# Kernel tuning notes

Hardware: AMD Instinct MI355X
Metric: run time of the kernel (lower is better)

Reference implementation:

```python
import jax, jax.numpy as jnp
import numpy as np

B, S, H = 4, 1024, 1024
R = 512          # num_rules
M = 1024         # memory_size
HEADS = 16
STEPS = 3        # inference_steps
TEMP = 1.0       # softmax_temperature
LN_EPS = 1e-5


def setup_inputs() -> dict:
    key = jax.random.key(0)
    ks = jax.random.split(key, 40)
    std = 0.02
    p = lambda k, shp: (jax.random.normal(k, shp, jnp.float32) * std)
    inp = {
        "hidden_states": jax.random.normal(ks[0], (B, S, H), jnp.float32),
        "rule_embeddings": p(ks[1], (R, H)),
        "rule_sel_w": p(ks[2], (H, R)), "rule_sel_b": jnp.zeros((R,), jnp.float32),
        # self-attention (nn.MultiheadAttention) projections
        "attn_wq": p(ks[3], (H, H)), "attn_bq": jnp.zeros((H,), jnp.float32),
        "attn_wk": p(ks[4], (H, H)), "attn_bk": jnp.zeros((H,), jnp.float32),
        "attn_wv": p(ks[5], (H, H)), "attn_bv": jnp.zeros((H,), jnp.float32),
        "attn_wo": p(ks[6], (H, H)), "attn_bo": jnp.zeros((H,), jnp.float32),
        # memory bank + key/query/value projections
        "memory": p(ks[7], (M, H)),
        "mem_q_w": p(ks[8], (H, H)), "mem_q_b": jnp.zeros((H,), jnp.float32),
        "mem_k_w": p(ks[9], (H, H)), "mem_k_b": jnp.zeros((H,), jnp.float32),
        "mem_v_w": p(ks[10], (H, H)), "mem_v_b": jnp.zeros((H,), jnp.float32),
        # memory_attention (nn.MultiheadAttention) projections
        "mattn_wq": p(ks[11], (H, H)), "mattn_bq": jnp.zeros((H,), jnp.float32),
        "mattn_wk": p(ks[12], (H, H)), "mattn_bk": jnp.zeros((H,), jnp.float32),
        "mattn_wv": p(ks[13], (H, H)), "mattn_bv": jnp.zeros((H,), jnp.float32),
        "mattn_wo": p(ks[14], (H, H)), "mattn_bo": jnp.zeros((H,), jnp.float32),
        # rule_application: Linear(2H,H)+LN+GELU+Linear(H,H)
        "ra_w1": p(ks[15], (2 * H, H)), "ra_b1": jnp.zeros((H,), jnp.float32),
        "ra_ln_s": jnp.ones((H,), jnp.float32), "ra_ln_b": jnp.zeros((H,), jnp.float32),
        "ra_w2": p(ks[16], (H, H)), "ra_b2": jnp.zeros((H,), jnp.float32),
        # confidence_scorer
        "conf_w": p(ks[17], (H, 1)), "conf_b": jnp.zeros((1,), jnp.float32),
    }
    return inp


def _mha(q_in, k_in, v_in, wq, bq, wk, bk, wv, bv, wo, bo):
    # standard nn.MultiheadAttention math (batch_first, eval mode -> no dropout)
    b, sq, h = q_in.shape
    d = h // HEADS
    qh = (q_in @ wq + bq).reshape(b, sq, HEADS, d)
    kh = (k_in @ wk + bk).reshape(b, -1, HEADS, d)
    vh = (v_in @ wv + bv).reshape(b, -1, HEADS, d)
    scores = jnp.einsum('bqhd,bkhd->bhqk', qh, kh) / jnp.sqrt(jnp.asarray(d, qh.dtype))
    probs = jax.nn.softmax(scores, axis=-1)
    out = jnp.einsum('bhqk,bkhd->bqhd', probs, vh).reshape(b, sq, h)
    return out @ wo + bo


def _ln(x, s, b):
    mu = x.mean(-1, keepdims=True)
    var = ((x - mu) ** 2).mean(-1, keepdims=True)
    return (x - mu) / jnp.sqrt(var + LN_EPS) * s + b


def reference(hidden_states, rule_embeddings, rule_sel_w, rule_sel_b,
              attn_wq, attn_bq, attn_wk, attn_bk, attn_wv, attn_bv, attn_wo, attn_bo,
              memory, mem_q_w, mem_q_b, mem_k_w, mem_k_b, mem_v_w, mem_v_b,
              mattn_wq, mattn_bq, mattn_wk, mattn_bk, mattn_wv, mattn_bv, mattn_wo, mattn_bo,
              ra_w1, ra_b1, ra_ln_s, ra_ln_b, ra_w2, ra_b2, conf_w, conf_b):
    h = hidden_states
    b = h.shape[0]
    # memory keys/values are input-independent: project once, broadcast over batch
    mk = jnp.broadcast_to((memory @ mem_k_w + mem_k_b)[None], (b, M, H))
    mv = jnp.broadcast_to((memory @ mem_v_w + mem_v_b)[None], (b, M, H))
    for _ in range(STEPS):
        # rule routing: soft selection over the rule-embedding table
        rule_probs = jax.nn.softmax((h @ rule_sel_w + rule_sel_b) / TEMP, axis=-1)  # [B,S,R]
        selected = jnp.einsum('bsr,rh->bsh', rule_probs, rule_embeddings)           # [B,S,H]
        # self-attention reasoning
        h = h + _mha(h, h, h, attn_wq, attn_bq, attn_wk, attn_bk,
                     attn_wv, attn_bv, attn_wo, attn_bo)
        # memory attention
        mq = h @ mem_q_w + mem_q_b
        h = h + _mha(mq, mk, mv, mattn_wq, mattn_bq, mattn_wk, mattn_bk,
                     mattn_wv, mattn_bv, mattn_wo, mattn_bo)
        # rule application MLP on [h ; selected_rules]
        x = jnp.concatenate([h, selected], axis=-1)                                  # [B,S,2H]
        u = jax.nn.gelu(_ln(x @ ra_w1 + ra_b1, ra_ln_s, ra_ln_b), approximate=False)
        h = h + (u @ ra_w2 + ra_b2)
    confidence = jax.nn.sigmoid(h @ conf_w + conf_b)  # [B,S,1]
    return h, confidence
```

## Files before the change

kernel.cpp:

```cpp
#include <hip/hip_runtime.h>
#include <stdint.h>

typedef _Float16 f16;
typedef __attribute__((ext_vector_type(4))) float floatx4;
typedef __attribute__((ext_vector_type(8))) f16   f16x8;
typedef __attribute__((ext_vector_type(4))) f16   f16x4;

#define GLD_LDS16(gp, lp)                                                                      \
  __builtin_amdgcn_global_load_lds((const __attribute__((address_space(1))) void*)(uintptr_t)(gp), \
                                   (__attribute__((address_space(3))) void*)(uintptr_t)(lp), 16, 0, 0)

struct SrlOut {
  int n0;
  const float* bias;
  const float* resid;
  float* Cf; f16* Cb;
  int ldcf, ldcb, transV;
  long long sCb, sCh;
};
struct SrlGemmArgs {
  const f16* A; const f16* B;
  int M, N, K, lda, ldb;
  long long sAb, sAh, sBb, sBh;
  float alpha;
  int nOuts;
  SrlOut out[4];
};

template<int BM, int BN, int MINW>
__global__ __launch_bounds__(256, MINW) void srl_gemm(SrlGemmArgs g) {
  constexpr int BK = 64;
  constexpr int ACH = BM / 32;
  constexpr int BCH = BN / 32;
  constexpr int MI  = (BM == 128 && BN == 128) ? 4 : 2;
  constexpr int NI  = (BN == 128) ? 4 : ((BM == 128) ? 4 : 2);
  __shared__ f16 As[BM * BK];
  __shared__ f16 Bs[BN * BK];
  const int tid  = threadIdx.x;
  const int wid  = tid >> 6;
  const int lane = tid & 63;
  const int z  = blockIdx.z, zh = z & 15, zb = z >> 4;

  const int gx = gridDim.x;
  const int NT = gx * gridDim.y;
  const int L  = blockIdx.y * gx + blockIdx.x;
  const int W  = ((NT & 7) == 0) ? ((L & 7) * (NT >> 3) + (L >> 3)) : L;
  const int tn = (W % gx) * BN;
  const int tm = (W / gx) * BM;

  const f16* Ab = g.A + (long long)zb * g.sAb + (long long)zh * g.sAh + (long long)tm * g.lda;
  const f16* Bb = g.B + (long long)zb * g.sBb + (long long)zh * g.sBh + (long long)tn * g.ldb;
  const int maxAr = g.M - 1 - tm;
  const int maxBr = g.N - 1 - tn;

  int aR[ACH], aO[ACH];
#pragma unroll
  for (int i = 0; i < ACH; ++i) {
    int e = wid * (BM * 16) + i * 512 + lane * 8;
    int r = e >> 6, s = (e >> 3) & 7;
    aR[i] = r; aO[i] = ((s - r) & 7) * 8;
  }
  int bR[BCH], bO[BCH];
#pragma unroll
  for (int i = 0; i < BCH; ++i) {
    int e = wid * (BN * 16) + i * 512 + lane * 8;
    int r = e >> 6, s = (e >> 3) & 7;
    bR[i] = r; bO[i] = ((s - r) & 7) * 8;
  }
  f16* lA = As + wid * (BM * 16);
  f16* lB = Bs + wid * (BN * 16);

  floatx4 acc[MI][NI];
#pragma unroll
  for (int a = 0; a < MI; ++a)
#pragma unroll
    for (int b = 0; b < NI; ++b) {
      acc[a][b][0] = 0.f; acc[a][b][1] = 0.f; acc[a][b][2] = 0.f; acc[a][b][3] = 0.f;
    }

  const int wm = (BM == 128 && BN == 128) ? (wid & 1) * 64
               : (BN == 128)              ? 0
               : (BM == 128)              ? wid * 32
                                          : (wid & 1) * 32;
  const int wn = (BM == 128 && BN == 128) ? (wid >> 1) * 64
               : (BM == 64 && BN == 64)   ? (wid >> 1) * 32
                                          : 0;
  const int lm = lane & 15;
  const int quad = lane >> 4;

  for (int k0 = 0; k0 < g.K; k0 += BK) {
    __syncthreads();
#pragma unroll
    for (int i = 0; i < ACH; ++i) {
      int r = aR[i] <= maxAr ? aR[i] : maxAr;
      GLD_LDS16(Ab + (long long)r * g.lda + (k0 + aO[i]), lA + i * 512);
    }
#pragma unroll
    for (int i = 0; i < BCH; ++i) {
      int r = bR[i] <= maxBr ? bR[i] : maxBr;
      GLD_LDS16(Bb + (long long)r * g.ldb + (k0 + bO[i]), lB + i * 512);
    }
    __syncthreads();
#pragma unroll
    for (int ks = 0; ks < 2; ++ks) {
      f16x8 af[MI], bfr[NI];
#pragma unroll
      for (int mi = 0; mi < MI; ++mi) {
        int row = wm + mi * 16 + lm;
        int sg = ((ks * 4 + quad) + row) & 7;
        af[mi] = *(const f16x8*)(As + row * 64 + sg * 8);
      }
#pragma unroll
      for (int ni = 0; ni < NI; ++ni) {
        int row = wn + ni * 16 + lm;
        int sg = ((ks * 4 + quad) + row) & 7;
        bfr[ni] = *(const f16x8*)(Bs + row * 64 + sg * 8);
      }
#pragma unroll
      for (int mi = 0; mi < MI; ++mi)
#pragma unroll
        for (int ni = 0; ni < NI; ++ni)
          acc[mi][ni] = __builtin_amdgcn_mfma_f32_16x16x32_f16(af[mi], bfr[ni], acc[mi][ni], 0, 0, 0);
    }
  }

  int oi = 0;
  for (int j = 1; j < g.nOuts; ++j)
    if (tn >= g.out[j].n0) oi = j;
  const SrlOut O = g.out[oi];
  const long long zc = (long long)zb * O.sCb + (long long)zh * O.sCh;
#pragma unroll
  for (int mi = 0; mi < MI; ++mi) {
#pragma unroll
    for (int r = 0; r < 4; ++r) {
      int m = tm + wm + mi * 16 + quad * 4 + r;
      if (m >= g.M) continue;
#pragma unroll
      for (int ni = 0; ni < NI; ++ni) {
        int n = tn + wn + ni * 16 + lm;
        if (n >= g.N) continue;
        int nl = n - O.n0;
        float v = acc[mi][ni][r] * g.alpha;
        if (O.bias)  v += O.bias[nl];
        if (O.resid) v += O.resid[(long long)m * O.ldcf + nl];
        if (O.Cf)    O.Cf[zc + (long long)m * O.ldcf + nl] = v;
        if (O.Cb) {
          long long idx = O.transV
              ? ((long long)(m >> 10) * 1048576 + (long long)nl * 1024 + (m & 1023))
              : (zc + (long long)m * O.ldcb + nl);
          O.Cb[idx] = (f16)v;
        }
      }
    }
  }
}

struct SrlFlashArgs {
  const f16* Q; const f16* K; const f16* VT; f16* O;
  long long sQb, sKb, sVb;
  float scale;
};

__global__ __launch_bounds__(256, 2) void srl_flash(SrlFlashArgs a) {
  __shared__ f16 Qs[8192];
  __shared__ f16 Ks[8192];
  __shared__ f16 VTs[8192];
  __shared__ f16 Ps[4][4096];
  const int tid = threadIdx.x, wid = tid >> 6, lane = tid & 63;
  const int quad = lane >> 4, c = lane & 15;
  const int L = blockIdx.x;
  const int bh = (L & 7) + ((L >> 6) << 3);
  const int qt = (L >> 3) & 7;
  const int b = bh >> 4, h = bh & 15;
  const f16* Qg = a.Q + (long long)b * a.sQb + (long long)qt * 131072 + h * 64;
  const f16* Kg = a.K + (long long)b * a.sKb + h * 64;
  const f16* Vg = a.VT + (long long)b * a.sVb + (long long)h * 65536;
  f16* Og = a.O + (long long)b * 1048576 + (long long)qt * 131072 + h * 64;

  int rRow[4], rOff[4];
#pragma unroll
  for (int i = 0; i < 4; ++i) {
    int e = wid * 2048 + i * 512 + lane * 8;
    int r = e >> 6, gL = (e >> 3) & 7;
    rRow[i] = r; rOff[i] = ((gL - r) & 7) * 8;
  }
  int vRow[4], vOff[4];
#pragma unroll
  for (int i = 0; i < 4; ++i) {
    int e = wid * 2048 + i * 512 + lane * 8;
    int d = e >> 7, gL = (e >> 3) & 15;
    vRow[i] = d; vOff[i] = ((gL - (d & 7)) & 15) * 8;
  }

#pragma unroll
  for (int i = 0; i < 4; ++i)
    GLD_LDS16(Qg + (long long)rRow[i] * 1024 + rOff[i], Qs + wid * 2048 + i * 512);
  __syncthreads();

  const int wq = wid * 32;
  f16x8 qf[2][2];
#pragma unroll
  for (int nf = 0; nf < 2; ++nf)
#pragma unroll
    for (int ch = 0; ch < 2; ++ch) {
      int row = wq + nf * 16 + c;
      int slot = ((ch * 4 + quad) + row) & 7;
      f16x8 v = *(const f16x8*)(Qs + row * 64 + slot * 8);
      f16 sc = (f16)a.scale;
#pragma unroll
      for (int j = 0; j < 8; ++j) v[j] = v[j] * sc;
      qf[nf][ch] = v;
    }

  float l_s[2] = {0.f, 0.f};
  floatx4 Oa[2][4];
#pragma unroll
  for (int nf = 0; nf < 2; ++nf)
#pragma unroll
    for (int no = 0; no < 4; ++no) {
      Oa[nf][no][0] = 0.f; Oa[nf][no][1] = 0.f; Oa[nf][no][2] = 0.f; Oa[nf][no][3] = 0.f;
    }

  for (int t = 0; t < 8; ++t) {
    __syncthreads();
#pragma unroll
    for (int i = 0; i < 4; ++i)
      GLD_LDS16(Kg + (long long)(t * 128 + rRow[i]) * 1024 + rOff[i], Ks + wid * 2048 + i * 512);
#pragma unroll
    for (int i = 0; i < 4; ++i)
      GLD_LDS16(Vg + (long long)vRow[i] * 1024 + (t * 128 + vOff[i]), VTs + wid * 2048 + i * 512);
    __syncthreads();

    floatx4 sT[2][8];
#pragma unroll
    for (int nf = 0; nf < 2; ++nf)
#pragma unroll
      for (int mf = 0; mf < 8; ++mf) {
        sT[nf][mf][0] = 0.f; sT[nf][mf][1] = 0.f; sT[nf][mf][2] = 0.f; sT[nf][mf][3] = 0.f;
      }
#pragma unroll
    for (int ch = 0; ch < 2; ++ch)
#pragma unroll
      for (int mf = 0; mf < 8; ++mf) {
        int key = mf * 16 + c;
        int slot = ((ch * 4 + quad) + key) & 7;
        f16x8 kf = *(const f16x8*)(Ks + key * 64 + slot * 8);
        sT[0][mf] = __builtin_amdgcn_mfma_f32_16x16x32_f16(kf, qf[0][ch], sT[0][mf], 0, 0, 0);
        sT[1][mf] = __builtin_amdgcn_mfma_f32_16x16x32_f16(kf, qf[1][ch], sT[1][mf], 0, 0, 0);
      }

#pragma unroll
    for (int nf = 0; nf < 2; ++nf) {
      float lt = 0.f;
      const int q = nf * 16 + c;
#pragma unroll
      for (int mf = 0; mf < 8; ++mf) {
        f16x4 pk;
#pragma unroll
        for (int r = 0; r < 4; ++r) {
          float p = __builtin_amdgcn_exp2f(sT[nf][mf][r]);
          lt += p;
          pk[r] = (f16)p;
        }
        int kg = mf * 2 + (quad >> 1), sub = (quad & 1) * 4;
        int slot = (kg + (q & 7)) & 15;
        *(f16x4*)(Ps[wid] + q * 128 + slot * 8 + sub) = pk;
      }
      lt += __shfl_xor(lt, 16);
      lt += __shfl_xor(lt, 32);
      l_s[nf] += lt;
    }
#pragma unroll
    for (int cc = 0; cc < 4; ++cc) {
      f16x8 af[2];
#pragma unroll
      for (int nf = 0; nf < 2; ++nf) {
        int q = nf * 16 + c;
        int slot = ((cc * 4 + quad) + (q & 7)) & 15;
        af[nf] = *(const f16x8*)(Ps[wid] + q * 128 + slot * 8);
      }
#pragma unroll
      for (int no = 0; no < 4; ++no) {
        int d = no * 16 + c;
        int slot = ((cc * 4 + quad) + (d & 7)) & 15;
        f16x8 vf = *(const f16x8*)(VTs + d * 128 + slot * 8);
        Oa[0][no] = __builtin_amdgcn_mfma_f32_16x16x32_f16(af[0], vf, Oa[0][no], 0, 0, 0);
        Oa[1][no] = __builtin_amdgcn_mfma_f32_16x16x32_f16(af[1], vf, Oa[1][no], 0, 0, 0);
      }
    }
  }

#pragma unroll
  for (int nf = 0; nf < 2; ++nf)
#pragma unroll
    for (int r = 0; r < 4; ++r) {
      float li = 1.f / __shfl(l_s[nf], quad * 4 + r);
      int qrow = wq + nf * 16 + quad * 4 + r;
#pragma unroll
      for (int no = 0; no < 4; ++no)
        Qs[qrow * 64 + no * 16 + c] = (f16)(Oa[nf][no][r] * li);
    }
  __syncthreads();
#pragma unroll
  for (int i = 0; i < 4; ++i) {
    int e = wid * 2048 + i * 512 + lane * 8;
    int row = e >> 6, col = e & 63;
    *(f16x8*)(Og + (long long)row * 1024 + col) = *(const f16x8*)(Qs + e);
  }
}

__global__ __launch_bounds__(256) void srl_softmax_rule(const float* logits, f16* probs) {
  __shared__ float red[16];
  const long long row = blockIdx.x;
  const float* p = logits + row * 512;
  const int tid = threadIdx.x;
  float v0 = p[tid], v1 = p[tid + 256];
  float mx = fmaxf(v0, v1);
#pragma unroll
  for (int o = 32; o > 0; o >>= 1) mx = fmaxf(mx, __shfl_down(mx, o));
  const int wid = tid >> 6, lane = tid & 63;
  if (lane == 0) red[wid] = mx;
  __syncthreads();
  if (tid == 0) red[8] = fmaxf(fmaxf(red[0], red[1]), fmaxf(red[2], red[3]));
  __syncthreads();
  mx = red[8];
  float e0 = __expf(v0 - mx), e1 = __expf(v1 - mx);
  float s = e0 + e1;
#pragma unroll
  for (int o = 32; o > 0; o >>= 1) s += __shfl_down(s, o);
  if (lane == 0) red[wid + 4] = s;
  __syncthreads();
  if (tid == 0) red[9] = 1.f / (red[4] + red[5] + red[6] + red[7]);
  __syncthreads();
  const float inv = red[9];
  probs[row * 512 + tid] = (f16)(e0 * inv);
  probs[row * 512 + tid + 256] = (f16)(e1 * inv);
}

__global__ __launch_bounds__(256) void srl_ln_gelu(const float* x, const float* gam, const float* bet, f16* out) {
  __shared__ float red[16];
  const long long row = blockIdx.x;
  const float* p = x + row * 1024;
  const int tid = threadIdx.x;
  float4 xv = *(const float4*)(p + tid * 4);
  float v[4] = {xv.x, xv.y, xv.z, xv.w};
  float s = v[0] + v[1] + v[2] + v[3];
  float s2 = v[0] * v[0] + v[1] * v[1] + v[2] * v[2] + v[3] * v[3];
#pragma unroll
  for (int o = 32; o > 0; o >>= 1) { s += __shfl_down(s, o); s2 += __shfl_down(s2, o); }
  const int wid = tid >> 6, lane = tid & 63;
  if (lane == 0) { red[wid] = s; red[wid + 4] = s2; }
  __syncthreads();
  if (tid == 0) {
    float ts = red[0] + red[1] + red[2] + red[3];
    float ts2 = red[4] + red[5] + red[6] + red[7];
    float mu = ts * (1.f / 1024.f);
    float var = ts2 * (1.f / 1024.f) - mu * mu;
    red[8] = mu;
    red[9] = rsqrtf(var + 1e-5f);
  }
  __syncthreads();
  const float mu = red[8], rstd = red[9];
  f16x4 o4;
#pragma unroll
  for (int i = 0; i < 4; ++i) {
    int c = tid * 4 + i;
    float t = (v[i] - mu) * rstd * gam[c] + bet[c];
    float ge = 0.5f * t * (1.f + erff(t * 0.70710678118654752f));
    o4[i] = (f16)ge;
  }
  *(f16x4*)(out + row * 1024 + tid * 4) = o4;
}

struct SrlTcEnt { const float* src; f16* dst; int rows, cols, trans, tileStart; };
struct SrlTcArgs { SrlTcEnt e[16]; };

__global__ __launch_bounds__(256) void srl_convert_weights(SrlTcArgs a) {
  __shared__ float t[32][33];
  const int bt = blockIdx.x;
  int ei = 0;
#pragma unroll
  for (int j = 1; j < 16; ++j)
    if (bt >= a.e[j].tileStart) ei = j;
  SrlTcEnt E = a.e[ei];
  const int lt = bt - E.tileStart;
  const int tcols = E.cols >> 5;
  const int tr = lt / tcols;
  const int tc = lt - tr * tcols;
  const int r = threadIdx.x >> 5;
  const int c = threadIdx.x & 31;
  if (!E.trans) {
#pragma unroll
    for (int p = 0; p < 4; ++p) {
      long long rr = tr * 32 + r + p * 8;
      long long idx = rr * E.cols + tc * 32 + c;
      E.dst[idx] = (f16)E.src[idx];
    }
  } else {
#pragma unroll
    for (int p = 0; p < 4; ++p)
      t[r + p * 8][c] = E.src[(long long)(tr * 32 + r + p * 8) * E.cols + tc * 32 + c];
    __syncthreads();
#pragma unroll
    for (int p = 0; p < 4; ++p)
      E.dst[(long long)(tc * 32 + r + p * 8) * E.rows + tr * 32 + c] = (f16)t[c][r + p * 8];
  }
}

__global__ __launch_bounds__(256) void srl_prep_bias(const float* rsel_b, const float* bq,
                                                     const float* bk, const float* bv,
                                                     const float* bmq, const float* maq_w,
                                                     const float* bmaq,
                                                     float* bias_qkvr, float* bcomp) {
  int i = blockIdx.x * 256 + threadIdx.x;
  if (i < 3584) {
    float v;
    if (i < 512) v = rsel_b[i];
    else if (i < 1536) v = bq[i - 512];
    else if (i < 2560) v = bk[i - 1536];
    else v = bv[i - 2560];
    bias_qkvr[i] = v;
  } else if (i < 3584 + 1024) {
    int m = i - 3584;
    float s = bmaq[m];
    for (int t = 0; t < 1024; ++t) s += bmq[t] * maq_w[(long long)t * 1024 + m];
    bcomp[m] = s;
  }
}

__global__ __launch_bounds__(256) void srl_h_init(const float* hidden, float* hf, f16* hx) {
  long long base = ((long long)blockIdx.x * 256 + threadIdx.x) * 4;
  float4 v = *(const float4*)(hidden + base);
  *(float4*)(hf + base) = v;
  long long row = base >> 10;
  int col = (int)(base & 1023);
  f16x4 b;
  b[0] = (f16)v.x; b[1] = (f16)v.y; b[2] = (f16)v.z; b[3] = (f16)v.w;
  *(f16x4*)(hx + row * 2048 + col) = b;
}

__global__ __launch_bounds__(256) void srl_finalize(const float* hf, const float* w, const float* b,
                                                    float* out, float* conf) {
  const int bid = blockIdx.x;
  if (bid < 4096) {
    long long base = ((long long)bid * 256 + threadIdx.x) * 4;
    *(float4*)(out + base) = *(const float4*)(hf + base);
  } else {
    const int row = (bid - 4096) * 4 + (threadIdx.x >> 6);
    const int lane = threadIdx.x & 63;
    const float* p = hf + (long long)row * 1024;
    float s = 0.f;
    for (int j = lane; j < 1024; j += 64) s += p[j] * w[j];
#pragma unroll
    for (int o = 32; o > 0; o >>= 1) s += __shfl_down(s, o);
    if (lane == 0) conf[row] = 1.f / (1.f + __expf(-(s + b[0])));
  }
}

extern "C" void kernel_launch(void* const* d_in, const int* in_sizes, int n_in,
                              void* d_out, int out_size, void* d_ws, size_t ws_size,
                              hipStream_t stream) {
  (void)in_sizes; (void)n_in; (void)out_size; (void)ws_size;
  const float* in_hidden   = (const float*)d_in[0];
  const float* in_rule_emb = (const float*)d_in[1];
  const float* in_rsel_w   = (const float*)d_in[2];
  const float* in_rsel_b   = (const float*)d_in[3];
  const float* in_attn_wq  = (const float*)d_in[4];
  const float* in_attn_bq  = (const float*)d_in[5];
  const float* in_attn_wk  = (const float*)d_in[6];
  const float* in_attn_bk  = (const float*)d_in[7];
  const float* in_attn_wv  = (const float*)d_in[8];
  const float* in_attn_bv  = (const float*)d_in[9];
  const float* in_attn_wo  = (const float*)d_in[10];
  const float* in_attn_bo  = (const float*)d_in[11];
  const float* in_memory   = (const float*)d_in[12];
  const float* in_mq_w     = (const float*)d_in[13];
  const float* in_mq_b     = (const float*)d_in[14];
  const float* in_mk_w     = (const float*)d_in[15];
  const float* in_mk_b     = (const float*)d_in[16];
  const float* in_mv_w     = (const float*)d_in[17];
  const float* in_mv_b     = (const float*)d_in[18];
  const float* in_maq_w    = (const float*)d_in[19];
  const float* in_maq_b    = (const float*)d_in[20];
  const float* in_mak_w    = (const float*)d_in[21];
  const float* in_mak_b    = (const float*)d_in[22];
  const float* in_mav_w    = (const float*)d_in[23];
  const float* in_mav_b    = (const float*)d_in[24];
  const float* in_mao_w    = (const float*)d_in[25];
  const float* in_mao_b    = (const float*)d_in[26];
  const float* in_ra_w1    = (const float*)d_in[27];
  const float* in_ra_b1    = (const float*)d_in[28];
  const float* in_ln_s     = (const float*)d_in[29];
  const float* in_ln_b     = (const float*)d_in[30];
  const float* in_ra_w2    = (const float*)d_in[31];
  const float* in_ra_b2    = (const float*)d_in[32];
  const float* in_conf_w   = (const float*)d_in[33];
  const float* in_conf_b   = (const float*)d_in[34];

  char* ws = (char*)d_ws;
  size_t off = 0;
  auto alloc = [&](size_t bytes) -> void* {
    void* p = ws + off;
    off = (off + bytes + 255) & ~(size_t)255;
    return p;
  };
  f16* wt_qkvr    = (f16*)alloc(3584 * 1024 * 2);
  float* bias_qkvr= (float*)alloc(3584 * 4);
  f16* wt_attn_o  = (f16*)alloc(1048576 * 2);
  f16* wt_mq_comp = (f16*)alloc(1048576 * 2);
  float* bcomp    = (float*)alloc(1024 * 4);
  f16* wt_mattn_o = (f16*)alloc(1048576 * 2);
  f16* wt_ra1     = (f16*)alloc(2097152 * 2);
  f16* wt_ra2     = (f16*)alloc(1048576 * 2);
  f16* wt_remb    = (f16*)alloc(524288 * 2);
  f16* wt_mem_kv  = (f16*)alloc(2097152 * 2);
  f16* wt_mattn_k = (f16*)alloc(1048576 * 2);
  f16* wt_mattn_v = (f16*)alloc(1048576 * 2);
  f16* mem_h      = (f16*)alloc(1048576 * 2);
  f16* mk_h       = (f16*)alloc(1048576 * 2);
  f16* mv_h       = (f16*)alloc(1048576 * 2);
  f16* mak_h      = (f16*)alloc(1048576 * 2);
  f16* mavT_h     = (f16*)alloc(1048576 * 2);
  float* h_f      = (float*)alloc(4194304 * 4);
  f16* hx         = (f16*)alloc(8388608 * 2);
  f16* q_h        = (f16*)alloc(4194304 * 2);
  f16* k_h        = (f16*)alloc(4194304 * 2);
  f16* vT_h       = (f16*)alloc(4194304 * 2);
  f16* ctx_h      = (f16*)alloc(4194304 * 2);
  f16* u_h        = (f16*)alloc(4194304 * 2);
  char* arena     = (char*)alloc(16777216);
  float* logits_f = (float*)arena;
  f16* probs_h    = (f16*)(arena + 8388608);
  float* ra1_f    = (float*)arena;
  f16* mqw_nt     = (f16*)arena;
  f16* wmaq_t     = (f16*)(arena + 2097152);

  auto mkOut = [](int n0, const float* bias, const float* resid, float* Cf, int ldcf,
                  f16* Cb, int ldcb, int transV, long long sCb, long long sCh) {
    SrlOut o;
    o.n0 = n0; o.bias = bias; o.resid = resid; o.Cf = Cf; o.Cb = Cb;
    o.ldcf = ldcf; o.ldcb = ldcb; o.transV = transV; o.sCb = sCb; o.sCh = sCh;
    return o;
  };
  auto runBig = [&](int M, int N, int K, const f16* A, int lda, const f16* B, int ldb,
                    float alpha, SrlGemmArgs g) {
    g.A = A; g.B = B; g.M = M; g.N = N; g.K = K; g.lda = lda; g.ldb = ldb;
    g.sAb = 0; g.sAh = 0; g.sBb = 0; g.sBh = 0; g.alpha = alpha;
    dim3 grid((N + 127) / 128, (M + 127) / 128, 1);
    hipLaunchKernelGGL((srl_gemm<128, 128, 2>), grid, dim3(256), 0, stream, g);
  };
  auto runSm1 = [&](int M, int N, int K, const f16* A, int lda, const f16* B, int ldb,
                    float alpha, const float* bias, const float* resid, float* Cf, int ldcf,
                    f16* Cb, int ldcb, int transV) {
    SrlGemmArgs g{};
    g.nOuts = 1;
    g.out[0] = mkOut(0, bias, resid, Cf, ldcf, Cb, ldcb, transV, 0, 0);
    g.A = A; g.B = B; g.M = M; g.N = N; g.K = K; g.lda = lda; g.ldb = ldb;
    g.sAb = 0; g.sAh = 0; g.sBb = 0; g.sBh = 0; g.alpha = alpha;
    dim3 grid((N + 63) / 64, (M + 63) / 64, 1);
    hipLaunchKernelGGL((srl_gemm<64, 64, 4>), grid, dim3(256), 0, stream, g);
  };
  auto runSm = [&](int M, int N, int K, const f16* A, int lda, const f16* B, int ldb,
                   float alpha, SrlGemmArgs g) {
    g.A = A; g.B = B; g.M = M; g.N = N; g.K = K; g.lda = lda; g.ldb = ldb;
    g.sAb = 0; g.sAh = 0; g.sBb = 0; g.sBh = 0; g.alpha = alpha;
    dim3 grid((N + 63) / 64, (M + 63) / 64, 1);
    hipLaunchKernelGGL((srl_gemm<64, 64, 4>), grid, dim3(256), 0, stream, g);
  };

  SrlTcArgs tc;
  int ts = 0;
  auto setent = [&](int i, const float* s, f16* d, int rows, int cols, int trans) {
    tc.e[i].src = s; tc.e[i].dst = d; tc.e[i].rows = rows; tc.e[i].cols = cols;
    tc.e[i].trans = trans; tc.e[i].tileStart = ts;
    ts += (rows / 32) * (cols / 32);
  };
  setent(0,  in_attn_wq, wt_qkvr + 512 * 1024, 1024, 1024, 1);
  setent(1,  in_attn_wk, wt_qkvr + 1536 * 1024, 1024, 1024, 1);
  setent(2,  in_attn_wv, wt_qkvr + 2560 * 1024, 1024, 1024, 1);
  setent(3,  in_rsel_w,  wt_qkvr, 1024, 512, 1);
  setent(4,  in_attn_wo, wt_attn_o, 1024, 1024, 1);
  setent(5,  in_mq_w,    mqw_nt, 1024, 1024, 0);
  setent(6,  in_maq_w,   wmaq_t, 1024, 1024, 1);
  setent(7,  in_mak_w,   wt_mattn_k, 1024, 1024, 1);
  setent(8,  in_mav_w,   wt_mattn_v, 1024, 1024, 1);
  setent(9,  in_mk_w,    wt_mem_kv, 1024, 1024, 1);
  setent(10, in_mv_w,    wt_mem_kv + 1048576, 1024, 1024, 1);
  setent(11, in_mao_w,   wt_mattn_o, 1024, 1024, 1);
  setent(12, in_ra_w1,   wt_ra1, 2048, 1024, 1);
  setent(13, in_ra_w2,   wt_ra2, 1024, 1024, 1);
  setent(14, in_rule_emb, wt_remb, 512, 1024, 1);
  setent(15, in_memory,  mem_h, 1024, 1024, 0);
  hipLaunchKernelGGL(srl_convert_weights, dim3(ts), dim3(256), 0, stream, tc);
  hipLaunchKernelGGL(srl_prep_bias, dim3(18), dim3(256), 0, stream,
                     in_rsel_b, in_attn_bq, in_attn_bk, in_attn_bv,
                     in_mq_b, in_maq_w, in_maq_b, bias_qkvr, bcomp);
  hipLaunchKernelGGL(srl_h_init, dim3(4096), dim3(256), 0, stream, in_hidden, h_f, hx);

  {
    SrlGemmArgs g{};
    g.nOuts = 2;
    g.out[0] = mkOut(0, in_mk_b, nullptr, nullptr, 0, mk_h, 1024, 0, 0, 0);
    g.out[1] = mkOut(1024, in_mv_b, nullptr, nullptr, 0, mv_h, 1024, 0, 0, 0);
    runSm(1024, 2048, 1024, mem_h, 1024, wt_mem_kv, 1024, 1.f, g);
  }
  runSm1(1024, 1024, 1024, mk_h, 1024, wt_mattn_k, 1024, 1.f, in_mak_b, nullptr, nullptr, 0, mak_h, 1024, 0);
  runSm1(1024, 1024, 1024, mv_h, 1024, wt_mattn_v, 1024, 1.f, in_mav_b, nullptr, nullptr, 0, mavT_h, 0, 1);
  runSm1(1024, 1024, 1024, wmaq_t, 1024, mqw_nt, 1024, 1.f, nullptr, nullptr, nullptr, 0, wt_mq_comp, 1024, 0);

  const float kLog2e = 1.4426950408889634f;
  for (int step = 0; step < 3; ++step) {
    {
      SrlGemmArgs g{};
      g.nOuts = 4;
      g.out[0] = mkOut(0,    bias_qkvr,        nullptr, logits_f, 512, nullptr, 0, 0, 0, 0);
      g.out[1] = mkOut(512,  bias_qkvr + 512,  nullptr, nullptr, 0, q_h, 1024, 0, 0, 0);
      g.out[2] = mkOut(1536, bias_qkvr + 1536, nullptr, nullptr, 0, k_h, 1024, 0, 0, 0);
      g.out[3] = mkOut(2560, bias_qkvr + 2560, nullptr, nullptr, 0, vT_h, 0, 1, 0, 0);
      runBig(4096, 3584, 1024, hx, 2048, wt_qkvr, 1024, 1.f, g);
    }
    hipLaunchKernelGGL(srl_softmax_rule, dim3(4096), dim3(256), 0, stream, logits_f, probs_h);
    runSm1(4096, 1024, 512, probs_h, 512, wt_remb, 512, 1.f, nullptr, nullptr, nullptr, 0, hx + 1024, 2048, 0);
    {
      SrlFlashArgs fa;
      fa.Q = q_h; fa.K = k_h; fa.VT = vT_h; fa.O = ctx_h;
      fa.sQb = 1048576; fa.sKb = 1048576; fa.sVb = 1048576; fa.scale = 0.125f * kLog2e;
      hipLaunchKernelGGL(srl_flash, dim3(512), dim3(256), 0, stream, fa);
    }
    runSm1(4096, 1024, 1024, ctx_h, 1024, wt_attn_o, 1024, 1.f, in_attn_bo, h_f, h_f, 1024, hx, 2048, 0);
    runSm1(4096, 1024, 1024, hx, 2048, wt_mq_comp, 1024, 1.f, bcomp, nullptr, nullptr, 0, k_h, 1024, 0);
    {
      SrlFlashArgs fa;
      fa.Q = k_h; fa.K = mak_h; fa.VT = mavT_h; fa.O = ctx_h;
      fa.sQb = 1048576; fa.sKb = 0; fa.sVb = 0; fa.scale = 0.125f * kLog2e;
      hipLaunchKernelGGL(srl_flash, dim3(512), dim3(256), 0, stream, fa);
    }
    runSm1(4096, 1024, 1024, ctx_h, 1024, wt_mattn_o, 1024, 1.f, in_mao_b, h_f, h_f, 1024, hx, 2048, 0);
    runSm1(4096, 1024, 2048, hx, 2048, wt_ra1, 2048, 1.f, in_ra_b1, nullptr, ra1_f, 1024, nullptr, 0, 0);
    hipLaunchKernelGGL(srl_ln_gelu, dim3(4096), dim3(256), 0, stream, ra1_f, in_ln_s, in_ln_b, u_h);
    runSm1(4096, 1024, 1024, u_h, 1024, wt_ra2, 1024, 1.f, in_ra_b2, h_f, h_f, 1024, hx, 2048, 0);
  }

  hipLaunchKernelGGL(srl_finalize, dim3(5120), dim3(256), 0, stream, h_f, in_conf_w, in_conf_b,
                     (float*)d_out, (float*)d_out + 4194304);
}
```

Measured before the change: 1.077 ms.

## Add 128x128 double-buffered direct-to-LDS GEMM kernel for per-step projections

Adds a new GEMM kernel using 512 threads and 128x128 tiles. It double-buffers K-tiles loaded straight into LDS with global_load_lds, uses an XOR-style swizzle to avoid bank conflicts, and remaps tiles in a grouped order for L2 locality. All per-step large GEMMs (the fused QKV/rule projection and the 4096-row output, memory-query and MLP projections) now use it instead of the 64x64 and old 128x128 kernels. It drops bounds checks and assumes M and N are multiples of 128 and the K-tile count is even.

```diff
diff --git a/kernel.cpp b/kernel.cpp
--- a/kernel.cpp
+++ b/kernel.cpp
@@ -148,6 +148,125 @@
           long long idx = O.transV
               ? ((long long)(m >> 10) * 1048576 + (long long)nl * 1024 + (m & 1023))
               : (zc + (long long)m * O.ldcb + nl);
+          O.Cb[idx] = (f16)v;
+        }
+      }
+    }
+  }
+}
+
+__global__ __launch_bounds__(512, 4) void srl_gemm_p(SrlGemmArgs g) {
+  __shared__ f16 As[2][8192];
+  __shared__ f16 Bs[2][8192];
+  const int tid  = threadIdx.x;
+  const int wid  = tid >> 6;
+  const int lane = tid & 63;
+
+  const int gx  = gridDim.x;
+  const int NTt = gx * gridDim.y;
+  const int L   = blockIdx.y * gx + blockIdx.x;
+  const int W   = ((NTt & 7) == 0) ? ((L & 7) * (NTt >> 3) + (L >> 3)) : L;
+  const int tn  = (W % gx) * 128;
+  const int tm  = (W / gx) * 128;
+
+  const f16* Ab = g.A + (long long)tm * g.lda;
+  const f16* Bb = g.B + (long long)tn * g.ldb;
+
+  int aR[2], aO[2];
+#pragma unroll
+  for (int i = 0; i < 2; ++i) {
+    int e = wid * 1024 + i * 512 + lane * 8;
+    int r = e >> 6, s = (e >> 3) & 7;
+    aR[i] = r; aO[i] = ((s - r) & 7) * 8;
+  }
+
+  const int wm = (wid >> 1) * 32;
+  const int wn = (wid & 1) * 64;
+  const int lm = lane & 15;
+  const int quad = lane >> 4;
+
+  floatx4 acc[2][4];
+#pragma unroll
+  for (int a = 0; a < 2; ++a)
+#pragma unroll
+    for (int b = 0; b < 4; ++b) {
+      acc[a][b][0] = 0.f; acc[a][b][1] = 0.f; acc[a][b][2] = 0.f; acc[a][b][3] = 0.f;
+    }
+
+  const int nk = g.K >> 6;
+
+  auto stage = [&](int kt, int bsel) {
+    const int k0 = kt << 6;
+    f16* lA = &As[bsel][0] + wid * 1024;
+    f16* lB = &Bs[bsel][0] + wid * 1024;
+#pragma unroll
+    for (int i = 0; i < 2; ++i)
+      GLD_LDS16(Ab + (long long)aR[i] * g.lda + (k0 + aO[i]), lA + i * 512);
+#pragma unroll
+    for (int i = 0; i < 2; ++i)
+      GLD_LDS16(Bb + (long long)aR[i] * g.ldb + (k0 + aO[i]), lB + i * 512);
+  };
+
+  stage(0, 0);
+  asm volatile("s_waitcnt vmcnt(0)" ::: "memory");
+  __builtin_amdgcn_s_barrier();
+
+  auto onestep = [&](int t, int cb) {
+    if (t + 1 < nk) stage(t + 1, cb ^ 1);
+    asm volatile("" ::: "memory");
+    const f16* Asb = &As[cb][0];
+    const f16* Bsb = &Bs[cb][0];
+#pragma unroll
+    for (int ks = 0; ks < 2; ++ks) {
+      f16x8 af[2], bfr[4];
+#pragma unroll
+      for (int mi = 0; mi < 2; ++mi) {
+        int row = wm + mi * 16 + lm;
+        int sg = ((ks * 4 + quad) + row) & 7;
+        af[mi] = *(const f16x8*)(Asb + row * 64 + sg * 8);
+      }
+#pragma unroll
+      for (int ni = 0; ni < 4; ++ni) {
+        int row = wn + ni * 16 + lm;
+        int sg = ((ks * 4 + quad) + row) & 7;
+        bfr[ni] = *(const f16x8*)(Bsb + row * 64 + sg * 8);
+      }
+#pragma unroll
+      for (int mi = 0; mi < 2; ++mi)
+#pragma unroll
+        for (int ni = 0; ni < 4; ++ni)
+          acc[mi][ni] = __builtin_amdgcn_mfma_f32_16x16x32_f16(af[mi], bfr[ni], acc[mi][ni], 0, 0, 0);
+    }
+    asm volatile("s_waitcnt vmcnt(0) lgkmcnt(0)" ::: "memory");
+    __builtin_amdgcn_s_barrier();
+  };
+
+  for (int t = 0; t < nk; t += 2) {
+    onestep(t, 0);
+    onestep(t + 1, 1);
+  }
+
+  int oi = 0;
+  for (int j = 1; j < g.nOuts; ++j)
+    if (tn >= g.out[j].n0) oi = j;
+  const SrlOut O = g.out[oi];
+#pragma unroll
+  for (int mi = 0; mi < 2; ++mi) {
+#pragma unroll
+    for (int r = 0; r < 4; ++r) {
+      int m = tm + wm + mi * 16 + quad * 4 + r;
+#pragma unroll
+      for (int ni = 0; ni < 4; ++ni) {
+        int n = tn + wn + ni * 16 + lm;
+        int nl = n - O.n0;
+        float v = acc[mi][ni][r] * g.alpha;
+        if (O.bias)  v += O.bias[nl];
+        if (O.resid) v += O.resid[(long long)m * O.ldcf + nl];
+        if (O.Cf)    O.Cf[(long long)m * O.ldcf + nl] = v;
+        if (O.Cb) {
+          long long idx = O.transV
+              ? ((long long)(m >> 10) * 1048576 + (long long)nl * 1024 + (m & 1023))
+              : ((long long)m * O.ldcb + nl);
           O.Cb[idx] = (f16)v;
         }
       }
@@ -542,12 +661,20 @@
     o.ldcf = ldcf; o.ldcb = ldcb; o.transV = transV; o.sCb = sCb; o.sCh = sCh;
     return o;
   };
-  auto runBig = [&](int M, int N, int K, const f16* A, int lda, const f16* B, int ldb,
-                    float alpha, SrlGemmArgs g) {
+  auto runP = [&](int M, int N, int K, const f16* A, int lda, const f16* B, int ldb,
+                  float alpha, SrlGemmArgs g) {
     g.A = A; g.B = B; g.M = M; g.N = N; g.K = K; g.lda = lda; g.ldb = ldb;
     g.sAb = 0; g.sAh = 0; g.sBb = 0; g.sBh = 0; g.alpha = alpha;
-    dim3 grid((N + 127) / 128, (M + 127) / 128, 1);
-    hipLaunchKernelGGL((srl_gemm<128, 128, 2>), grid, dim3(256), 0, stream, g);
+    dim3 grid(N / 128, M / 128, 1);
+    hipLaunchKernelGGL(srl_gemm_p, grid, dim3(512), 0, stream, g);
+  };
+  auto runP1 = [&](int M, int N, int K, const f16* A, int lda, const f16* B, int ldb,
+                   float alpha, const float* bias, const float* resid, float* Cf, int ldcf,
+                   f16* Cb, int ldcb, int transV) {
+    SrlGemmArgs g{};
+    g.nOuts = 1;
+    g.out[0] = mkOut(0, bias, resid, Cf, ldcf, Cb, ldcb, transV, 0, 0);
+    runP(M, N, K, A, lda, B, ldb, alpha, g);
   };
   auto runSm1 = [&](int M, int N, int K, const f16* A, int lda, const f16* B, int ldb,
                     float alpha, const float* bias, const float* resid, float* Cf, int ldcf,
@@ -617,28 +744,28 @@
       g.out[1] = mkOut(512,  bias_qkvr + 512,  nullptr, nullptr, 0, q_h, 1024, 0, 0, 0);
       g.out[2] = mkOut(1536, bias_qkvr + 1536, nullptr, nullptr, 0, k_h, 1024, 0, 0, 0);
       g.out[3] = mkOut(2560, bias_qkvr + 2560, nullptr, nullptr, 0, vT_h, 0, 1, 0, 0);
-      runBig(4096, 3584, 1024, hx, 2048, wt_qkvr, 1024, 1.f, g);
+      runP(4096, 3584, 1024, hx, 2048, wt_qkvr, 1024, 1.f, g);
     }
     hipLaunchKernelGGL(srl_softmax_rule, dim3(4096), dim3(256), 0, stream, logits_f, probs_h);
-    runSm1(4096, 1024, 512, probs_h, 512, wt_remb, 512, 1.f, nullptr, nullptr, nullptr, 0, hx + 1024, 2048, 0);
+    runP1(4096, 1024, 512, probs_h, 512, wt_remb, 512, 1.f, nullptr, nullptr, nullptr, 0, hx + 1024, 2048, 0);
     {
       SrlFlashArgs fa;
       fa.Q = q_h; fa.K = k_h; fa.VT = vT_h; fa.O = ctx_h;
       fa.sQb = 1048576; fa.sKb = 1048576; fa.sVb = 1048576; fa.scale = 0.125f * kLog2e;
       hipLaunchKernelGGL(srl_flash, dim3(512), dim3(256), 0, stream, fa);
     }
-    runSm1(4096, 1024, 1024, ctx_h, 1024, wt_attn_o, 1024, 1.f, in_attn_bo, h_f, h_f, 1024, hx, 2048, 0);
-    runSm1(4096, 1024, 1024, hx, 2048, wt_mq_comp, 1024, 1.f, bcomp, nullptr, nullptr, 0, k_h, 1024, 0);
+    runP1(4096, 1024, 1024, ctx_h, 1024, wt_attn_o, 1024, 1.f, in_attn_bo, h_f, h_f, 1024, hx, 2048, 0);
+    runP1(4096, 1024, 1024, hx, 2048, wt_mq_comp, 1024, 1.f, bcomp, nullptr, nullptr, 0, k_h, 1024, 0);
     {
       SrlFlashArgs fa;
       fa.Q = k_h; fa.K = mak_h; fa.VT = mavT_h; fa.O = ctx_h;
       fa.sQb = 1048576; fa.sKb = 0; fa.sVb = 0; fa.scale = 0.125f * kLog2e;
       hipLaunchKernelGGL(srl_flash, dim3(512), dim3(256), 0, stream, fa);
     }
-    runSm1(4096, 1024, 1024, ctx_h, 1024, wt_mattn_o, 1024, 1.f, in_mao_b, h_f, h_f, 1024, hx, 2048, 0);
-    runSm1(4096, 1024, 2048, hx, 2048, wt_ra1, 2048, 1.f, in_ra_b1, nullptr, ra1_f, 1024, nullptr, 0, 0);
+    runP1(4096, 1024, 1024, ctx_h, 1024, wt_mattn_o, 1024, 1.f, in_mao_b, h_f, h_f, 1024, hx, 2048, 0);
+    runP1(4096, 1024, 2048, hx, 2048, wt_ra1, 2048, 1.f, in_ra_b1, nullptr, ra1_f, 1024, nullptr, 0, 0);
     hipLaunchKernelGGL(srl_ln_gelu, dim3(4096), dim3(256), 0, stream, ra1_f, in_ln_s, in_ln_b, u_h);
-    runSm1(4096, 1024, 1024, u_h, 1024, wt_ra2, 1024, 1.f, in_ra_b2, h_f, h_f, 1024, hx, 2048, 0);
+    runP1(4096, 1024, 1024, u_h, 1024, wt_ra2, 1024, 1.f, in_ra_b2, h_f, h_f, 1024, hx, 2048, 0);
   }
 
   hipLaunchKernelGGL(srl_finalize, dim3(5120), dim3(256), 0, stream, h_f, in_conf_w, in_conf_b,
```

After: 1.154 ms. 7.2% more time.
